# Performance work log

Measured on AMD Instinct MI355X. Metric: run time of the kernel, lower is better.

Reference implementation:

```python
import jax, jax.numpy as jnp
import numpy as np

N_NODES = 100000
IN_DIM = 512
OUT_DIM = 16
N_EDGES = 3200000


def setup_inputs() -> dict:
    key = jax.random.key(0)
    k1, k2, k3, k4 = jax.random.split(key, 4)
    x = jax.random.normal(k1, (N_NODES, IN_DIM), dtype=jnp.float32)
    edge_index = jax.random.randint(k2, (2, N_EDGES), 0, N_NODES, dtype=jnp.int64)
    # GCNConv params (glorot weight, zero bias as in PyG)
    scale = jnp.sqrt(6.0 / (IN_DIM + OUT_DIM)).astype(jnp.float32)
    W = jax.random.uniform(k3, (IN_DIM, OUT_DIM), dtype=jnp.float32, minval=-scale, maxval=scale)
    b = jnp.zeros((OUT_DIM,), dtype=jnp.float32)
    return {"x": x, "edge_index": edge_index, "W": W, "b": b}


def reference(x, edge_index, W, b):
    n = x.shape[0]
    # GCNConv with normalize=True: add self-loops, symmetric deg normalization
    loops = jnp.arange(n, dtype=edge_index.dtype)
    row = jnp.concatenate([edge_index[0], loops])  # source nodes
    col = jnp.concatenate([edge_index[1], loops])  # target nodes

    h = x @ W  # [N, 16] dense linear transform

    deg = jax.ops.segment_sum(jnp.ones_like(col, dtype=h.dtype), col, num_segments=n)
    dinv = jnp.where(deg > 0, jax.lax.rsqrt(jnp.maximum(deg, 1.0)), 0.0)
    norm = dinv[row] * dinv[col]  # [E+N]

    # gather source features, scale, scatter-add into targets
    out = jax.ops.segment_sum(norm[:, None] * h[row], col, num_segments=n)
    return out + b
```

## Files before the change

kernel.cpp:

```cpp
#include <hip/hip_runtime.h>
#include <hip/hip_fp16.h>

#define IN_DIM 512
#define OUT_DIM 16
#define KC 32
#define TILE_ROWS 256

#define BSHIFT 8
#define BNODES 256
#define MAXBUCK 512
#define BIN_CHUNK 4096

__global__ __launch_bounds__(256) void gemm_xw(const float* __restrict__ x,
                                               const float* __restrict__ W,
                                               const int* __restrict__ hist,
                                               __half* __restrict__ hp, int n) {
    __shared__ float xs[TILE_ROWS * (KC + 1)];
    const int tid = threadIdx.x;
    const int rbase = blockIdx.x * TILE_ROWS;
    const int myrow = rbase + tid;

    float acc[OUT_DIM];
#pragma unroll
    for (int j = 0; j < OUT_DIM; ++j) acc[j] = 0.f;

    for (int kc = 0; kc < IN_DIM; kc += KC) {
        __syncthreads();
#pragma unroll
        for (int i = 0; i < 8; ++i) {
            const int v = tid + 256 * i;
            const int r = v >> 3;
            const int c = (v & 7) << 2;
            if (rbase + r < n) {
                const float4 f = *(const float4*)(x + (size_t)(rbase + r) * IN_DIM + kc + c);
                float* d = xs + r * (KC + 1) + c;
                d[0] = f.x; d[1] = f.y; d[2] = f.z; d[3] = f.w;
            }
        }
        __syncthreads();

        const float* xrow = xs + tid * (KC + 1);
#pragma unroll 4
        for (int k = 0; k < KC; ++k) {
            const float xv = xrow[k];
            const float* wr = W + (size_t)(kc + k) * OUT_DIM;
            const float4 w0 = *(const float4*)(wr + 0);
            const float4 w1 = *(const float4*)(wr + 4);
            const float4 w2 = *(const float4*)(wr + 8);
            const float4 w3 = *(const float4*)(wr + 12);
            acc[0]  += xv * w0.x; acc[1]  += xv * w0.y; acc[2]  += xv * w0.z; acc[3]  += xv * w0.w;
            acc[4]  += xv * w1.x; acc[5]  += xv * w1.y; acc[6]  += xv * w1.z; acc[7]  += xv * w1.w;
            acc[8]  += xv * w2.x; acc[9]  += xv * w2.y; acc[10] += xv * w2.z; acc[11] += xv * w2.w;
            acc[12] += xv * w3.x; acc[13] += xv * w3.y; acc[14] += xv * w3.z; acc[15] += xv * w3.w;
        }
    }

    if (myrow < n) {
        const float s = rsqrtf((float)(hist[myrow] + 1));
        __half2* op = (__half2*)(hp + (size_t)myrow * OUT_DIM);
#pragma unroll
        for (int j = 0; j < 8; ++j)
            op[j] = __floats2half2_rn(s * acc[2 * j], s * acc[2 * j + 1]);
    }
}

__device__ inline void scan512_excl(const int* src, int* dst, int lane) {
    int c[8], pre[8];
    int tot = 0;
#pragma unroll
    for (int k = 0; k < 8; ++k) { c[k] = src[lane * 8 + k]; pre[k] = tot; tot += c[k]; }
    int incl = tot;
#pragma unroll
    for (int d = 1; d < 64; d <<= 1) {
        const int u = __shfl_up(incl, d);
        if (lane >= d) incl += u;
    }
    const int excl = incl - tot;
#pragma unroll
    for (int k = 0; k < 8; ++k) dst[lane * 8 + k] = excl + pre[k];
}

__device__ inline void scan256_excl(const int* src, int* dst, int lane) {
    int c[4], pre[4];
    int tot = 0;
#pragma unroll
    for (int k = 0; k < 4; ++k) { c[k] = src[lane * 4 + k]; pre[k] = tot; tot += c[k]; }
    int incl = tot;
#pragma unroll
    for (int d = 1; d < 64; d <<= 1) {
        const int u = __shfl_up(incl, d);
        if (lane >= d) incl += u;
    }
    const int excl = incl - tot;
#pragma unroll
    for (int k = 0; k < 4; ++k) dst[lane * 4 + k] = excl + pre[k];
}

__global__ __launch_bounds__(256) void bcount(const int* __restrict__ dst,
                                              int* __restrict__ bcnt, int E, int nbuck) {
    __shared__ int lhist[MAXBUCK];
    const int tid = threadIdx.x;
    for (int i = tid; i < MAXBUCK; i += 256) lhist[i] = 0;
    __syncthreads();

    const int base = blockIdx.x * BIN_CHUNK + tid * 16;
#pragma unroll
    for (int g = 0; g < 4; ++g) {
        const int e = base + g * 4;
        if (e + 3 < E) {
            const int4 d = *(const int4*)(dst + e);
            atomicAdd(&lhist[d.x >> BSHIFT], 1);
            atomicAdd(&lhist[d.y >> BSHIFT], 1);
            atomicAdd(&lhist[d.z >> BSHIFT], 1);
            atomicAdd(&lhist[d.w >> BSHIFT], 1);
        } else {
            for (int u = 0; u < 4; ++u)
                if (e + u < E) atomicAdd(&lhist[dst[e + u] >> BSHIFT], 1);
        }
    }
    __syncthreads();
    for (int i = tid; i < nbuck; i += 256)
        if (lhist[i] > 0) atomicAdd(&bcnt[i], lhist[i]);
}

__global__ __launch_bounds__(512) void bucket_scan(const int* __restrict__ bcnt,
                                                   int* __restrict__ bbase,
                                                   int* __restrict__ bcur, int nbuck) {
    __shared__ int sm[MAXBUCK];
    const int t = threadIdx.x;
    sm[t] = (t < nbuck) ? bcnt[t] : 0;
    __syncthreads();
    if (t < 64) scan512_excl(sm, sm, t);
    __syncthreads();
    bbase[t] = sm[t];
    bcur[t] = sm[t];
}

__global__ __launch_bounds__(256) void bin_edges(const int* __restrict__ ei,
                                                 int* __restrict__ bcur,
                                                 int* __restrict__ bins,
                                                 int E, int nbuck) {
    __shared__ int lhist[MAXBUCK];
    __shared__ int lbase[MAXBUCK];
    __shared__ int gbase[MAXBUCK];
    __shared__ int stage[BIN_CHUNK];
    __shared__ short sbkt[BIN_CHUNK];

    const int tid = threadIdx.x;
    const int e0 = blockIdx.x * BIN_CHUNK;
    const int cnt = min(BIN_CHUNK, E - e0);

    for (int i = tid; i < MAXBUCK; i += 256) lhist[i] = 0;
    __syncthreads();

    int myb[16], myr[16], myp[16];
    const int base = e0 + tid * 16;
#pragma unroll
    for (int g = 0; g < 4; ++g) {
        const int e = base + g * 4;
        int ss[4], dd[4];
        if ((E & 3) == 0 && e + 3 < E) {
            const int4 s4 = *(const int4*)(ei + e);
            const int4 d4 = *(const int4*)(ei + (size_t)E + e);
            ss[0] = s4.x; ss[1] = s4.y; ss[2] = s4.z; ss[3] = s4.w;
            dd[0] = d4.x; dd[1] = d4.y; dd[2] = d4.z; dd[3] = d4.w;
        } else {
#pragma unroll
            for (int u = 0; u < 4; ++u) {
                const int idx = e + u;
                ss[u] = (idx < E) ? ei[idx] : -1;
                dd[u] = (idx < E) ? ei[(size_t)E + idx] : 0;
            }
        }
#pragma unroll
        for (int u = 0; u < 4; ++u) {
            const int j = g * 4 + u;
            if (ss[u] >= 0) {
                const int bk = dd[u] >> BSHIFT;
                myb[j] = bk;
                myp[j] = (ss[u] << BSHIFT) | (dd[u] & (BNODES - 1));
                myr[j] = atomicAdd(&lhist[bk], 1);
            } else {
                myb[j] = -1; myr[j] = 0; myp[j] = 0;
            }
        }
    }
    __syncthreads();

    if (tid < 64) scan512_excl(lhist, lbase, tid);
    for (int i = tid; i < nbuck; i += 256)
        if (lhist[i] > 0) gbase[i] = atomicAdd(&bcur[i], lhist[i]);
    __syncthreads();

#pragma unroll
    for (int j = 0; j < 16; ++j) {
        if (myb[j] >= 0) {
            const int p = lbase[myb[j]] + myr[j];
            stage[p] = myp[j];
            sbkt[p] = (short)myb[j];
        }
    }
    __syncthreads();

    for (int i = tid; i < cnt; i += 256) {
        const int bk = sbkt[i];
        bins[gbase[bk] + (i - lbase[bk])] = stage[i];
    }
}

__global__ __launch_bounds__(256) void bucket_sort(const int* __restrict__ bins,
                                                   const int* __restrict__ bbase,
                                                   const int* __restrict__ bcur,
                                                   int* __restrict__ csr,
                                                   int* __restrict__ hist,
                                                   int* __restrict__ off, int n) {
    __shared__ int nhist[BNODES];
    __shared__ int nbase[BNODES];
    __shared__ int ncur[BNODES];
    const int tid = threadIdx.x;
    const int b = blockIdx.x;
    const int s = bbase[b];
    const int e = bcur[b];

    nhist[tid] = 0;
    __syncthreads();
    for (int i = s + tid; i < e; i += 256)
        atomicAdd(&nhist[bins[i] & (BNODES - 1)], 1);
    __syncthreads();
    if (tid < 64) scan256_excl(nhist, nbase, tid);
    __syncthreads();

    const int node = (b << BSHIFT) + tid;
    if (node < n) {
        hist[node] = nhist[tid];
        off[node] = s + nbase[tid];
    }
    ncur[tid] = nbase[tid];
    __syncthreads();

    for (int i = s + tid; i < e; i += 256) {
        const int p = bins[i];
        const int r = atomicAdd(&ncur[p & (BNODES - 1)], 1);
        csr[s + r] = p >> BSHIFT;
    }
}

__global__ __launch_bounds__(256) void gather_out(const int* __restrict__ csr,
                                                  const int* __restrict__ off,
                                                  const int* __restrict__ hist,
                                                  const __half* __restrict__ hp,
                                                  const float* __restrict__ b,
                                                  float* __restrict__ out, int n) {
    const long long gid = (long long)blockIdx.x * 256 + threadIdx.x;
    const int d = (int)(gid >> 3);
    const int j2 = (int)(gid & 7);
    if (d >= n) return;

    const int base = off[d];
    const int deg = hist[d];
    const __half2* hpt = (const __half2*)hp;

    const __half2 sv = hpt[(size_t)d * 8 + j2];
    float ax = __low2float(sv), ay = __high2float(sv);

    int k = 0;
    for (; k + 4 <= deg; k += 4) {
        const int s0 = csr[base + k + 0];
        const int s1 = csr[base + k + 1];
        const int s2 = csr[base + k + 2];
        const int s3 = csr[base + k + 3];
        const __half2 v0 = hpt[(size_t)s0 * 8 + j2];
        const __half2 v1 = hpt[(size_t)s1 * 8 + j2];
        const __half2 v2 = hpt[(size_t)s2 * 8 + j2];
        const __half2 v3 = hpt[(size_t)s3 * 8 + j2];
        ax += __low2float(v0) + __low2float(v1) + __low2float(v2) + __low2float(v3);
        ay += __high2float(v0) + __high2float(v1) + __high2float(v2) + __high2float(v3);
    }
    for (; k < deg; ++k) {
        const __half2 v = hpt[(size_t)csr[base + k] * 8 + j2];
        ax += __low2float(v);
        ay += __high2float(v);
    }

    const float di = rsqrtf((float)(deg + 1));
    float2 o;
    o.x = di * ax + b[2 * j2];
    o.y = di * ay + b[2 * j2 + 1];
    ((float2*)out)[(size_t)d * 8 + j2] = o;
}

__global__ void hist_dst(const int* __restrict__ dst, int* __restrict__ hist, int E) {
    const int t = blockIdx.x * 256 + threadIdx.x;
    const int e0 = t * 4;
    if ((E & 3) == 0 && e0 + 3 < E) {
        const int4 d = *(const int4*)(dst + e0);
        atomicAdd(&hist[d.x], 1);
        atomicAdd(&hist[d.y], 1);
        atomicAdd(&hist[d.z], 1);
        atomicAdd(&hist[d.w], 1);
    } else {
        for (int e = e0; e < E && e < e0 + 4; ++e) atomicAdd(&hist[dst[e]], 1);
    }
}

__global__ __launch_bounds__(256) void scatter_f16(const int* __restrict__ ei,
                                                   const __half* __restrict__ hp,
                                                   __half2* __restrict__ acc, int E) {
    const long long gid = (long long)blockIdx.x * 256 + threadIdx.x;
    const int g = (int)(gid >> 3);
    const int j2 = (int)(gid & 7);
    const int e0 = g * 4;
    if (e0 >= E) return;

    int src[4], dst[4];
#pragma unroll
    for (int u = 0; u < 4; ++u) {
        const int e = e0 + u;
        src[u] = (e < E) ? ei[e] : -1;
        dst[u] = (e < E) ? ei[(size_t)E + e] : -1;
    }
    __half2 v[4];
#pragma unroll
    for (int u = 0; u < 4; ++u)
        if (src[u] >= 0) v[u] = ((const __half2*)(hp + (size_t)src[u] * OUT_DIM))[j2];
#pragma unroll
    for (int u = 0; u < 4; ++u)
        if (dst[u] >= 0) unsafeAtomicAdd(&acc[(size_t)dst[u] * 8 + j2], v[u]);
}

__global__ void finalize(const __half* __restrict__ acc, const __half* __restrict__ hp,
                         const int* __restrict__ hist, const float* __restrict__ b,
                         float* __restrict__ out, int n) {
    const int gid = blockIdx.x * 256 + threadIdx.x;
    if (gid >= n * OUT_DIM) return;
    const int i = gid >> 4;
    const int j = gid & 15;
    const float di = rsqrtf((float)(hist[i] + 1));
    out[gid] = di * (__half2float(acc[gid]) + __half2float(hp[gid])) + b[j];
}


extern "C" void kernel_launch(void* const* d_in, const int* in_sizes, int n_in,
                              void* d_out, int out_size, void* d_ws, size_t ws_size,
                              hipStream_t stream) {
    const float* x  = (const float*)d_in[0];
    const int*   ei = (const int*)d_in[1];
    const float* W  = (const float*)d_in[2];
    const float* b  = (const float*)d_in[3];
    float* out = (float*)d_out;

    const int n = in_sizes[0] / IN_DIM;
    const int E = in_sizes[1] / 2;
    const int nbuck = (n + BNODES - 1) >> BSHIFT;

    __half* hp    = (__half*)d_ws;
    int*    hist  = (int*)(hp + (size_t)n * OUT_DIM);
    int*    off   = hist + n;
    int*    bbase = off + n;
    int*    bcur  = bbase + MAXBUCK;
    int*    bcnt  = bcur + MAXBUCK;
    int*    bins  = bcnt + MAXBUCK;
    int*    csr   = bins + (size_t)E;

    const size_t need = (size_t)n * OUT_DIM * sizeof(__half)
                      + ((size_t)2 * n + 3 * MAXBUCK) * sizeof(int)
                      + 2 * (size_t)E * sizeof(int);

    if (ws_size >= need && nbuck <= MAXBUCK && n < (1 << 23)) {
        hipMemsetAsync(bcnt, 0, MAXBUCK * sizeof(int), stream);

        bcount<<<(E + BIN_CHUNK - 1) / BIN_CHUNK, 256, 0, stream>>>(ei + E, bcnt, E, nbuck);
        bucket_scan<<<1, 512, 0, stream>>>(bcnt, bbase, bcur, nbuck);
        bin_edges<<<(E + BIN_CHUNK - 1) / BIN_CHUNK, 256, 0, stream>>>(ei, bcur, bins, E, nbuck);
        bucket_sort<<<nbuck, 256, 0, stream>>>(bins, bbase, bcur, csr, hist, off, n);
        gemm_xw<<<(n + TILE_ROWS - 1) / TILE_ROWS, 256, 0, stream>>>(x, W, hist, hp, n);
        gather_out<<<(int)(((size_t)n * 8 + 255) / 256), 256, 0, stream>>>(csr, off, hist, hp, b, out, n);
    } else {
        __half* acc = (__half*)(hist + n);
        hipMemsetAsync(hist, 0, (size_t)n * sizeof(int), stream);
        hipMemsetAsync(acc, 0, (size_t)n * OUT_DIM * sizeof(__half), stream);

        hist_dst<<<(E + 1023) / 1024, 256, 0, stream>>>(ei + E, hist, E);
        gemm_xw<<<(n + TILE_ROWS - 1) / TILE_ROWS, 256, 0, stream>>>(x, W, hist, hp, n);
        const long long st = ((long long)(E + 3) / 4) * 8;
        scatter_f16<<<(int)((st + 255) / 256), 256, 0, stream>>>(ei, hp, (__half2*)acc, E);
        finalize<<<(n * OUT_DIM + 255) / 256, 256, 0, stream>>>(acc, hp, hist, b, out, n);
    }
}
```

Baseline: 456.2 us.

## Split GEMM K dimension across four wavefronts with shared-memory reduction

Adds a GEMM variant where each block handles 64 rows and its four wavefronts each cover a quarter of the 512-wide K dimension, then combines the partial sums through LDS. Block count rises from n/256 to n/64, giving more parallelism for the memory-bound read of x on a GPU with many CUs. The cost is an extra LDS reduction step and only one wave doing the final normalize-and-store. The per-load access pattern also changes: each row's quarter chunks are 128-byte segments spread across the row.

```diff
diff --git a/kernel.cpp b/kernel.cpp
--- a/kernel.cpp
+++ b/kernel.cpp
@@ -10,6 +10,79 @@
 #define BNODES 256
 #define MAXBUCK 512
 #define BIN_CHUNK 4096
+
+__global__ __launch_bounds__(256) void gemm_xw_split(const float* __restrict__ x,
+                                                     const float* __restrict__ W,
+                                                     const int* __restrict__ hist,
+                                                     __half* __restrict__ hp, int n) {
+    __shared__ float xs[4 * 64 * (KC + 1)];
+    const int tid = threadIdx.x;
+    const int r = tid & 63;
+    const int q = __builtin_amdgcn_readfirstlane(tid >> 6);
+    const int rbase = blockIdx.x * 64;
+    const int myrow = rbase + r;
+
+    float acc[OUT_DIM];
+#pragma unroll
+    for (int j = 0; j < OUT_DIM; ++j) acc[j] = 0.f;
+
+    for (int c = 0; c < 4; ++c) {
+        __syncthreads();
+#pragma unroll
+        for (int i = 0; i < 8; ++i) {
+            const int v = tid + 256 * i;
+            const int row = v >> 5;
+            const int c4 = v & 31;
+            const int qq = c4 >> 3;
+            const int f4 = (c4 & 7) << 2;
+            if (rbase + row < n) {
+                const float4 f = *(const float4*)(x + (size_t)(rbase + row) * IN_DIM
+                                                  + qq * 128 + c * KC + f4);
+                float* d = xs + qq * (64 * (KC + 1)) + row * (KC + 1) + f4;
+                d[0] = f.x; d[1] = f.y; d[2] = f.z; d[3] = f.w;
+            }
+        }
+        __syncthreads();
+
+        const float* xrow = xs + q * (64 * (KC + 1)) + r * (KC + 1);
+        const float* Wb = W + (size_t)(q * 128 + c * KC) * OUT_DIM;
+#pragma unroll 4
+        for (int k = 0; k < KC; ++k) {
+            const float xv = xrow[k];
+            const float* wr = Wb + k * OUT_DIM;
+            const float4 w0 = *(const float4*)(wr + 0);
+            const float4 w1 = *(const float4*)(wr + 4);
+            const float4 w2 = *(const float4*)(wr + 8);
+            const float4 w3 = *(const float4*)(wr + 12);
+            acc[0]  += xv * w0.x; acc[1]  += xv * w0.y; acc[2]  += xv * w0.z; acc[3]  += xv * w0.w;
+            acc[4]  += xv * w1.x; acc[5]  += xv * w1.y; acc[6]  += xv * w1.z; acc[7]  += xv * w1.w;
+            acc[8]  += xv * w2.x; acc[9]  += xv * w2.y; acc[10] += xv * w2.z; acc[11] += xv * w2.w;
+            acc[12] += xv * w3.x; acc[13] += xv * w3.y; acc[14] += xv * w3.z; acc[15] += xv * w3.w;
+        }
+    }
+
+    __syncthreads();
+    float* red = xs;
+    if (q > 0) {
+        float* d = red + (q - 1) * (64 * 17) + r * 17;
+#pragma unroll
+        for (int j = 0; j < OUT_DIM; ++j) d[j] = acc[j];
+    }
+    __syncthreads();
+    if (tid < 64 && myrow < n) {
+        const float* p0 = red + 0 * (64 * 17) + tid * 17;
+        const float* p1 = red + 1 * (64 * 17) + tid * 17;
+        const float* p2 = red + 2 * (64 * 17) + tid * 17;
+        const float s = rsqrtf((float)(hist[myrow] + 1));
+        __half2* op = (__half2*)(hp + (size_t)myrow * OUT_DIM);
+#pragma unroll
+        for (int j = 0; j < 8; ++j) {
+            const float lo = acc[2 * j]     + p0[2 * j]     + p1[2 * j]     + p2[2 * j];
+            const float hi = acc[2 * j + 1] + p0[2 * j + 1] + p1[2 * j + 1] + p2[2 * j + 1];
+            op[j] = __floats2half2_rn(s * lo, s * hi);
+        }
+    }
+}
 
 __global__ __launch_bounds__(256) void gemm_xw(const float* __restrict__ x,
                                                const float* __restrict__ W,
@@ -373,7 +446,7 @@
         bucket_scan<<<1, 512, 0, stream>>>(bcnt, bbase, bcur, nbuck);
         bin_edges<<<(E + BIN_CHUNK - 1) / BIN_CHUNK, 256, 0, stream>>>(ei, bcur, bins, E, nbuck);
         bucket_sort<<<nbuck, 256, 0, stream>>>(bins, bbase, bcur, csr, hist, off, n);
-        gemm_xw<<<(n + TILE_ROWS - 1) / TILE_ROWS, 256, 0, stream>>>(x, W, hist, hp, n);
+        gemm_xw_split<<<(n + 63) / 64, 256, 0, stream>>>(x, W, hist, hp, n);
         gather_out<<<(int)(((size_t)n * 8 + 255) / 256), 256, 0, stream>>>(csr, off, hist, hp, b, out, n);
     } else {
         __half* acc = (__half*)(hist + n);
```

Measured after the change: 420.4 us. 7.9% less time.

## Add wave-private double-buffered GEMM and widen bucket_sort blocks to 1024 threads

Applied to the files above, without the earlier changes.

Replaces the block-synchronous x@W tile kernel with a per-wavefront GEMM. Each wave stages its own 64 rows into private shared memory and double-buffers global loads in registers, so the block-wide barriers go away and loads overlap compute. bucket_sort now runs 1024 threads per bucket to give more parallelism on the per-bucket histogram and scatter. The bcount chunk size gets its own constant but keeps the same value. The wave kernel has no explicit intra-wave sync and holds more registers, which may lower occupancy.

```diff
diff --git a/kernel.cpp b/kernel.cpp
--- a/kernel.cpp
+++ b/kernel.cpp
@@ -9,7 +9,93 @@
 #define BSHIFT 8
 #define BNODES 256
 #define MAXBUCK 512
+#define BCOUNT_CHUNK 4096
 #define BIN_CHUNK 4096
+
+__global__ __launch_bounds__(256) void gemm_wave(const float* __restrict__ x,
+                                                 const float* __restrict__ W,
+                                                 const int* __restrict__ hist,
+                                                 __half* __restrict__ hp, int n) {
+    __shared__ float xs[4 * 64 * (KC + 1)];
+    const int tid = threadIdx.x;
+    const int lane = tid & 63;
+    const int wid = __builtin_amdgcn_readfirstlane(tid >> 6);
+    const int rbase = blockIdx.x * 256 + wid * 64;
+    if (rbase >= n) return;
+    const int myrow = rbase + lane;
+
+    float* xw = xs + wid * (64 * (KC + 1));
+    const int srow = lane >> 3;
+    const int scol = (lane & 7) << 2;
+
+    float4 stA[8], stB[8];
+
+#define LOADC(buf, c)                                                          \
+    {                                                                          \
+        _Pragma("unroll")                                                      \
+        for (int i = 0; i < 8; ++i) {                                          \
+            const int rr = rbase + 8 * i + srow;                               \
+            if (rr < n)                                                        \
+                buf[i] = *(const float4*)(x + (size_t)rr * IN_DIM + (c) * KC + scol); \
+            else                                                               \
+                buf[i] = make_float4(0.f, 0.f, 0.f, 0.f);                      \
+        }                                                                      \
+    }
+
+#define STOREC(buf)                                                            \
+    {                                                                          \
+        _Pragma("unroll")                                                      \
+        for (int i = 0; i < 8; ++i) {                                          \
+            float* d = xw + (8 * i + srow) * (KC + 1) + scol;                  \
+            d[0] = buf[i].x; d[1] = buf[i].y; d[2] = buf[i].z; d[3] = buf[i].w; \
+        }                                                                      \
+    }
+
+#define COMPUTEC(c)                                                            \
+    {                                                                          \
+        const float* xrow = xw + lane * (KC + 1);                              \
+        const float* Wb = W + (size_t)(c) * KC * OUT_DIM;                      \
+        _Pragma("unroll 4")                                                    \
+        for (int k = 0; k < KC; ++k) {                                         \
+            const float xv = xrow[k];                                          \
+            const float* wr = Wb + k * OUT_DIM;                                \
+            const float4 w0 = *(const float4*)(wr + 0);                        \
+            const float4 w1 = *(const float4*)(wr + 4);                        \
+            const float4 w2 = *(const float4*)(wr + 8);                        \
+            const float4 w3 = *(const float4*)(wr + 12);                       \
+            acc[0]  += xv * w0.x; acc[1]  += xv * w0.y; acc[2]  += xv * w0.z; acc[3]  += xv * w0.w; \
+            acc[4]  += xv * w1.x; acc[5]  += xv * w1.y; acc[6]  += xv * w1.z; acc[7]  += xv * w1.w; \
+            acc[8]  += xv * w2.x; acc[9]  += xv * w2.y; acc[10] += xv * w2.z; acc[11] += xv * w2.w; \
+            acc[12] += xv * w3.x; acc[13] += xv * w3.y; acc[14] += xv * w3.z; acc[15] += xv * w3.w; \
+        }                                                                      \
+    }
+
+    float acc[OUT_DIM];
+#pragma unroll
+    for (int j = 0; j < OUT_DIM; ++j) acc[j] = 0.f;
+
+    LOADC(stA, 0);
+    for (int cc = 0; cc < 8; ++cc) {
+        const int c0 = 2 * cc, c1 = 2 * cc + 1;
+        STOREC(stA);
+        LOADC(stB, c1);
+        COMPUTEC(c0);
+        STOREC(stB);
+        if (c1 + 1 < 16) LOADC(stA, c1 + 1);
+        COMPUTEC(c1);
+    }
+
+    if (myrow < n) {
+        const float s = rsqrtf((float)(hist[myrow] + 1));
+        __half2* op = (__half2*)(hp + (size_t)myrow * OUT_DIM);
+#pragma unroll
+        for (int j = 0; j < 8; ++j)
+            op[j] = __floats2half2_rn(s * acc[2 * j], s * acc[2 * j + 1]);
+    }
+#undef LOADC
+#undef STOREC
+#undef COMPUTEC
+}
 
 __global__ __launch_bounds__(256) void gemm_xw(const float* __restrict__ x,
                                                const float* __restrict__ W,
@@ -103,7 +189,7 @@
     for (int i = tid; i < MAXBUCK; i += 256) lhist[i] = 0;
     __syncthreads();
 
-    const int base = blockIdx.x * BIN_CHUNK + tid * 16;
+    const int base = blockIdx.x * BCOUNT_CHUNK + tid * 16;
 #pragma unroll
     for (int g = 0; g < 4; ++g) {
         const int e = base + g * 4;
@@ -208,12 +294,12 @@
     }
 }
 
-__global__ __launch_bounds__(256) void bucket_sort(const int* __restrict__ bins,
-                                                   const int* __restrict__ bbase,
-                                                   const int* __restrict__ bcur,
-                                                   int* __restrict__ csr,
-                                                   int* __restrict__ hist,
-                                                   int* __restrict__ off, int n) {
+__global__ __launch_bounds__(1024) void bucket_sort(const int* __restrict__ bins,
+                                                    const int* __restrict__ bbase,
+                                                    const int* __restrict__ bcur,
+                                                    int* __restrict__ csr,
+                                                    int* __restrict__ hist,
+                                                    int* __restrict__ off, int n) {
     __shared__ int nhist[BNODES];
     __shared__ int nbase[BNODES];
     __shared__ int ncur[BNODES];
@@ -222,23 +308,25 @@
     const int s = bbase[b];
     const int e = bcur[b];
 
-    nhist[tid] = 0;
-    __syncthreads();
-    for (int i = s + tid; i < e; i += 256)
+    if (tid < BNODES) nhist[tid] = 0;
+    __syncthreads();
+    for (int i = s + tid; i < e; i += 1024)
         atomicAdd(&nhist[bins[i] & (BNODES - 1)], 1);
     __syncthreads();
     if (tid < 64) scan256_excl(nhist, nbase, tid);
     __syncthreads();
 
-    const int node = (b << BSHIFT) + tid;
-    if (node < n) {
-        hist[node] = nhist[tid];
-        off[node] = s + nbase[tid];
-    }
-    ncur[tid] = nbase[tid];
-    __syncthreads();
-
-    for (int i = s + tid; i < e; i += 256) {
+    if (tid < BNODES) {
+        const int node = (b << BSHIFT) + tid;
+        if (node < n) {
+            hist[node] = nhist[tid];
+            off[node] = s + nbase[tid];
+        }
+        ncur[tid] = nbase[tid];
+    }
+    __syncthreads();
+
+    for (int i = s + tid; i < e; i += 1024) {
         const int p = bins[i];
         const int r = atomicAdd(&ncur[p & (BNODES - 1)], 1);
         csr[s + r] = p >> BSHIFT;
@@ -369,11 +457,11 @@
     if (ws_size >= need && nbuck <= MAXBUCK && n < (1 << 23)) {
         hipMemsetAsync(bcnt, 0, MAXBUCK * sizeof(int), stream);
 
-        bcount<<<(E + BIN_CHUNK - 1) / BIN_CHUNK, 256, 0, stream>>>(ei + E, bcnt, E, nbuck);
+        bcount<<<(E + BCOUNT_CHUNK - 1) / BCOUNT_CHUNK, 256, 0, stream>>>(ei + E, bcnt, E, nbuck);
         bucket_scan<<<1, 512, 0, stream>>>(bcnt, bbase, bcur, nbuck);
         bin_edges<<<(E + BIN_CHUNK - 1) / BIN_CHUNK, 256, 0, stream>>>(ei, bcur, bins, E, nbuck);
-        bucket_sort<<<nbuck, 256, 0, stream>>>(bins, bbase, bcur, csr, hist, off, n);
-        gemm_xw<<<(n + TILE_ROWS - 1) / TILE_ROWS, 256, 0, stream>>>(x, W, hist, hp, n);
+        bucket_sort<<<nbuck, 1024, 0, stream>>>(bins, bbase, bcur, csr, hist, off, n);
+        gemm_wave<<<(n + 255) / 256, 256, 0, stream>>>(x, W, hist, hp, n);
         gather_out<<<(int)(((size_t)n * 8 + 255) / 256), 256, 0, stream>>>(csr, off, hist, hp, b, out, n);
     } else {
         __half* acc = (__half*)(hist + n);
```

Result: faster. 428.3 us (-6.1%).
